# Performance work log

Hardware: AMD Instinct MI355X
Metric: run time of the kernel (lower is better)

## Reference

```python
import jax, jax.numpy as jnp
import numpy as np

HEAD_SIZE = 128


def setup_inputs() -> dict:
    key = jax.random.key(0)
    k0, k1, k2, k3 = jax.random.split(key, 4)
    B, S, E, H = 4, 4096, 1024, HEAD_SIZE
    x = jax.random.normal(k0, (B, S, E), dtype=jnp.float32)
    scale = 1.0 / np.sqrt(E).astype(np.float32)
    Wq = jax.random.normal(k1, (E, H), dtype=jnp.float32) * scale
    Wk = jax.random.normal(k2, (E, H), dtype=jnp.float32) * scale
    Wv = jax.random.normal(k3, (E, H), dtype=jnp.float32) * scale
    k_mask = jnp.ones((B, S), dtype=jnp.int32)
    return {"x": x, "Wq": Wq, "Wk": Wk, "Wv": Wv, "k_mask": k_mask}


def reference(x, Wq, Wk, Wv, k_mask):
    # Self-attention path (kv=None), causal=True
    Q = x @ Wq  # [B, S, H]
    K = x @ Wk  # [B, S, H]
    V = x @ Wv  # [B, S, H]
    inv_sqrt_h = np.float32(1.0 / np.sqrt(HEAD_SIZE))
    att = jnp.einsum('bqh,bkh->bqk', Q, K) * inv_sqrt_h  # [B, S, S]
    neg_inf = jnp.float32(-jnp.inf)
    # padding mask over keys: [B, 1, S_k]
    att = jnp.where(k_mask[:, None, :] == 0, neg_inf, att)
    # causal mask: tril over (q_len, k_len)
    S = Q.shape[1]
    c_mask = jnp.tril(jnp.ones((S, S), dtype=bool))  # [S, S]
    att = jnp.where(c_mask[None, :, :], att, neg_inf)
    att = jax.nn.softmax(att, axis=-1)
    return att @ V  # [B, S, H]
```

## Files before the change

kernel.cpp:

```cpp
#include <hip/hip_runtime.h>
#include <hip/hip_bf16.h>

typedef unsigned short u16;
typedef __attribute__((ext_vector_type(8))) short bf16x8;
typedef __attribute__((ext_vector_type(4))) float f32x4;
typedef __attribute__((ext_vector_type(4))) unsigned short u16x4;

#define SQ 4096
#define HQ 128
#define NCHUNK 144

__device__ __forceinline__ u16 f2b(float f) {
  unsigned int u = __float_as_uint(f);
  unsigned int r = (u + 0x7fffu + ((u >> 16) & 1u)) >> 16;
  return (u16)r;
}

__device__ __forceinline__ u16 f2b_fast(float f) {
  __hip_bfloat16 h = __float2bfloat16(f);
  return __builtin_bit_cast(u16, h);
}

__device__ __forceinline__ float b2f(u16 v) {
  unsigned int u = ((unsigned int)v) << 16;
  return __uint_as_float(u);
}

__device__ __forceinline__ void gload_lds16(const u16* gsrc, u16* ldst) {
  __builtin_amdgcn_global_load_lds((const __attribute__((address_space(1))) void*)gsrc,
                                   (__attribute__((address_space(3))) void*)ldst, 16, 0, 0);
}

__global__ __launch_bounds__(256) void k_wt(const float* __restrict__ Wq, const float* __restrict__ Wk,
                                            const float* __restrict__ Wv, u16* __restrict__ wt) {
  int idx = blockIdx.x * 256 + threadIdx.x;
  int z = idx >> 17, r = idx & 131071, n = r >> 10, k = r & 1023;
  const float* W = (z == 0) ? Wq : (z == 1) ? Wk : Wv;
  wt[idx] = f2b(W[k * 128 + n]);
}

__global__ __launch_bounds__(512, 4) void k_proj(const float* __restrict__ x, const u16* __restrict__ wt,
                                                 u16* __restrict__ qb, u16* __restrict__ kb,
                                                 u16* __restrict__ vt) {
  int mt = blockIdx.x, nh = blockIdx.y;
  int t = threadIdx.x;
  int w = t >> 6, lane = t & 63;
  int wm = w >> 2, wn = w & 3;
  int lr = lane & 15, lg = lane >> 4;

  __shared__ __align__(16) u16 xl[2][64 * 32];
  __shared__ __align__(16) u16 wl[2][192 * 32];

  int srow = t >> 3, sc8 = t & 7;
  const float* xg = x + (long)(mt * 64 + srow) * 1024 + sc8 * 4;
  int xch = ((sc8 >> 1) ^ ((srow >> 1) & 3));
  int xoff = srow * 32 + xch * 8 + (sc8 & 1) * 4;

  f32x4 acc[2][3];
#pragma unroll
  for (int i = 0; i < 2; ++i)
#pragma unroll
    for (int j = 0; j < 3; ++j) acc[i][j] = (f32x4){0.f, 0.f, 0.f, 0.f};

  const u16* wbase = wt + (long)(nh * 192) * 1024;

  auto stage_w = [&](int bufi, int k0) {
#pragma unroll
    for (int i = 0; i < 2; ++i) {
      int ci = i * 512 + t;
      if (ci < 768) {
        int row = ci >> 2, ch = ci & 3;
        gload_lds16(wbase + (long)row * 1024 + k0 + ((ch ^ ((row >> 1) & 3)) << 3),
                    &wl[bufi][0] + ci * 8);
      }
    }
  };

  auto xwrite = [&](int bufi, float4 a, float4 b2) {
    u16x4 o0, o1;
    o0[0] = f2b_fast(a.x); o0[1] = f2b_fast(a.y); o0[2] = f2b_fast(a.z); o0[3] = f2b_fast(a.w);
    o1[0] = f2b_fast(b2.x); o1[1] = f2b_fast(b2.y); o1[2] = f2b_fast(b2.z); o1[3] = f2b_fast(b2.w);
    *(u16x4*)(&xl[bufi][0] + xoff) = (sc8 & 1) ? o0 : o0;
  };

  {
    float4 a0 = *(const float4*)(xg);
    stage_w(0, 0);
    u16x4 o;
    o[0] = f2b_fast(a0.x); o[1] = f2b_fast(a0.y); o[2] = f2b_fast(a0.z); o[3] = f2b_fast(a0.w);
    *(u16x4*)(&xl[0][0] + xoff) = o;
  }
  float4 p0 = *(const float4*)(xg + 32);
  float4 p1 = *(const float4*)(xg + 64);
  __syncthreads();

  for (int ks = 0; ks < 32; ++ks) {
    int cur = ks & 1;
    float4 p2;
    if (ks + 3 < 32) p2 = *(const float4*)(xg + (ks + 3) * 32);
    if (ks + 1 < 32) {
      stage_w(cur ^ 1, (ks + 1) * 32);
      u16x4 o;
      o[0] = f2b_fast(p0.x); o[1] = f2b_fast(p0.y); o[2] = f2b_fast(p0.z); o[3] = f2b_fast(p0.w);
      *(u16x4*)(&xl[cur ^ 1][0] + xoff) = o;
    }
    bf16x8 af[2], bfr[3];
#pragma unroll
    for (int i = 0; i < 2; ++i) {
      int row = wm * 32 + i * 16 + lr;
      af[i] = *(const bf16x8*)(&xl[cur][0] + row * 32 + ((lg ^ ((row >> 1) & 3)) << 3));
    }
#pragma unroll
    for (int j = 0; j < 3; ++j) {
      int row = wn * 48 + j * 16 + lr;
      bfr[j] = *(const bf16x8*)(&wl[cur][0] + row * 32 + ((lg ^ ((row >> 1) & 3)) << 3));
    }
#pragma unroll
    for (int i = 0; i < 2; ++i)
#pragma unroll
      for (int j = 0; j < 3; ++j)
        acc[i][j] = __builtin_amdgcn_mfma_f32_16x16x32_bf16(af[i], bfr[j], acc[i][j], 0, 0, 0);
    p0 = p1; p1 = p2;
    __syncthreads();
  }

#pragma unroll
  for (int i = 0; i < 2; ++i)
#pragma unroll
    for (int j = 0; j < 3; ++j)
#pragma unroll
      for (int r = 0; r < 4; ++r) {
        int m = mt * 64 + wm * 32 + i * 16 + lg * 4 + r;
        int col = nh * 192 + wn * 48 + j * 16 + lr;
        int z = col >> 7, cz = col & 127;
        u16 v = f2b(acc[i][j][r]);
        if (z == 0) qb[(long)m * 128 + cz] = v;
        else if (z == 1) kb[(long)m * 128 + cz] = v;
        else { int bb = m >> 12, sR = m & 4095; vt[(long)bb * 524288 + (long)cz * 4096 + sR] = v; }
      }
}

__global__ __launch_bounds__(512, 4) void k_attn(const u16* __restrict__ qb, const u16* __restrict__ kb,
                                                 const u16* __restrict__ vt, const int* __restrict__ kmask,
                                                 u16* __restrict__ po, float* __restrict__ pl) {
  const float SCALE_LOG2 = 0.08838834764831845f * 1.4426950408889634f;
  const float MFIX = 24.0f;
  int f = (NCHUNK - 1) - (int)blockIdx.x;
  int b = blockIdx.y;
  int qt2 = 0, cum = 0;
  while (cum + ((qt2 + 4) >> 2) <= f) { cum += (qt2 + 4) >> 2; ++qt2; }
  int kc = f - cum;
  int ntile = 2 * qt2 + 2;
  int kt0 = kc * 8;
  int kt1 = min(kt0 + 8, ntile);

  int t = threadIdx.x, w = t >> 6, lane = t & 63;
  int lr = lane & 15, lg = lane >> 4, sw = lr & 7;
  int qrow0 = qt2 * 128 + w * 16;
  const u16* Q = qb + ((long)(b * SQ + qrow0)) * HQ;
  const u16* K = kb + (long)b * SQ * HQ;
  const u16* V = vt + (long)b * HQ * SQ;
  const int* msk = kmask + b * SQ;

  __shared__ __align__(16) u16 Kl[2][64 * 128];
  __shared__ __align__(16) u16 Vl[2][128 * 64];
  __shared__ __align__(16) u16 plds[8][16 * 64];

  bf16x8 aq[4];
#pragma unroll
  for (int c = 0; c < 4; ++c) aq[c] = *(const bf16x8*)(Q + lr * HQ + c * 32 + lg * 8);

  bf16x8 ones;
#pragma unroll
  for (int e = 0; e < 8; ++e) ones[e] = (short)0x3F80;

  f32x4 o[8];
#pragma unroll
  for (int n = 0; n < 8; ++n) o[n] = (f32x4){0.f, 0.f, 0.f, 0.f};
  f32x4 l_acc = (f32x4){0.f, 0.f, 0.f, 0.f};

  auto stage = [&](int bufi, int kb0) {
    const u16* Kg = K + (long)kb0 * HQ;
    const u16* Vg = V + kb0;
#pragma unroll
    for (int i = 0; i < 2; ++i) {
      int ci = w * 2 + i;
      int o16 = ci * 64 + lane;
      int row = o16 >> 4, ch = o16 & 15;
      gload_lds16(Kg + row * HQ + ((ch ^ (row & 7)) << 3), &Kl[bufi][ci * 512]);
    }
#pragma unroll
    for (int i = 0; i < 2; ++i) {
      int ci = w * 2 + i;
      int o16 = ci * 64 + lane;
      int row = o16 >> 3, ch = o16 & 7;
      gload_lds16(Vg + (long)row * SQ + ((ch ^ (row & 7)) << 3), &Vl[bufi][ci * 512]);
    }
  };

  stage(0, kt0 * 64);
  __syncthreads();

  u16* pw = &plds[w][0];
  for (int kt = kt0; kt < kt1; ++kt) {
    int cur = (kt - kt0) & 1;
    int kb0 = kt * 64;
    if (kt + 1 < kt1) stage(cur ^ 1, kb0 + 64);

    if (kb0 <= qrow0 + 15) {
      f32x4 s[4];
#pragma unroll
      for (int h = 0; h < 4; ++h) {
        f32x4 acc = (f32x4){0.f, 0.f, 0.f, 0.f};
        const u16* Kp = &Kl[cur][(h * 16 + lr) * 128];
#pragma unroll
        for (int c = 0; c < 4; ++c) {
          bf16x8 bk = *(const bf16x8*)(Kp + (((c * 4 + lg) ^ sw) << 3));
          acc = __builtin_amdgcn_mfma_f32_16x16x32_bf16(aq[c], bk, acc, 0, 0, 0);
        }
        s[h] = acc;
      }
      float mf[4];
#pragma unroll
      for (int h = 0; h < 4; ++h) mf[h] = (msk[kb0 + h * 16 + lr] != 0) ? 1.0f : 0.0f;
      bool needc = (kb0 + 63 > qrow0);
#pragma unroll
      for (int r = 0; r < 4; ++r) {
        int row = lg * 4 + r;
        int qr = qrow0 + row;
#pragma unroll
        for (int h = 0; h < 4; ++h) {
          float p = __builtin_exp2f(fmaf(s[h][r], SCALE_LOG2, -MFIX)) * mf[h];
          if (needc) p = ((kb0 + h * 16 + lr) <= qr) ? p : 0.0f;
          int poff = row * 64 + ((((h * 2 + (lr >> 3)) ^ (row & 7))) << 3) + (lr & 7);
          pw[poff] = f2b_fast(p);
        }
      }
      bf16x8 ap0 = *(const bf16x8*)(pw + lr * 64 + ((lg ^ sw) << 3));
      bf16x8 ap1 = *(const bf16x8*)(pw + lr * 64 + (((4 + lg) ^ sw) << 3));
      l_acc = __builtin_amdgcn_mfma_f32_16x16x32_bf16(ap0, ones, l_acc, 0, 0, 0);
      l_acc = __builtin_amdgcn_mfma_f32_16x16x32_bf16(ap1, ones, l_acc, 0, 0, 0);
#pragma unroll
      for (int n = 0; n < 8; ++n) {
        const u16* Vp = &Vl[cur][(n * 16 + lr) * 64];
        bf16x8 bv0 = *(const bf16x8*)(Vp + ((lg ^ sw) << 3));
        bf16x8 bv1 = *(const bf16x8*)(Vp + (((4 + lg) ^ sw) << 3));
        o[n] = __builtin_amdgcn_mfma_f32_16x16x32_bf16(ap0, bv0, o[n], 0, 0, 0);
        o[n] = __builtin_amdgcn_mfma_f32_16x16x32_bf16(ap1, bv1, o[n], 0, 0, 0);
      }
    }
    __syncthreads();
  }

  long p = (long)b * NCHUNK + f;
  u16* pob = po + p * 16384;
#pragma unroll
  for (int n = 0; n < 8; ++n)
#pragma unroll
    for (int r = 0; r < 4; ++r)
      pob[(w * 16 + lg * 4 + r) * 128 + n * 16 + lr] = f2b_fast(o[n][r]);
  if (lr == 0) {
#pragma unroll
    for (int r = 0; r < 4; ++r) pl[p * 128 + w * 16 + lg * 4 + r] = l_acc[r];
  }
}

__global__ __launch_bounds__(256) void k_merge(const u16* __restrict__ po, const float* __restrict__ pl,
                                               float* __restrict__ out) {
  int qt2 = blockIdx.x, b = blockIdx.y;
  int nch = (qt2 + 4) >> 2;
  int pre = 0;
  for (int q = 0; q < qt2; ++q) pre += (q + 4) >> 2;
  long pbase = (long)b * NCHUNK + pre;
  int t = threadIdx.x;
  int row = t >> 1, c0 = (t & 1) * 64;
  float l = 0.f;
  for (int i = 0; i < nch; ++i) l += pl[(pbase + i) * 128 + row];
  float inv = 1.0f / l;
  const u16* p0 = po + pbase * 16384 + row * 128 + c0;
  float* orow = out + ((long)(b * SQ + qt2 * 128 + row)) * HQ + c0;
#pragma unroll
  for (int j = 0; j < 64; j += 4) {
    float acc0 = 0.f, acc1 = 0.f, acc2 = 0.f, acc3 = 0.f;
    for (int i = 0; i < nch; ++i) {
      u16x4 v = *(const u16x4*)(p0 + (long)i * 16384 + j);
      acc0 += b2f(v[0]); acc1 += b2f(v[1]); acc2 += b2f(v[2]); acc3 += b2f(v[3]);
    }
    float4 r = {acc0 * inv, acc1 * inv, acc2 * inv, acc3 * inv};
    *(float4*)(orow + j) = r;
  }
}

extern "C" void kernel_launch(void* const* d_in, const int* in_sizes, int n_in,
                              void* d_out, int out_size, void* d_ws, size_t ws_size,
                              hipStream_t stream) {
  const float* x  = (const float*)d_in[0];
  const float* Wq = (const float*)d_in[1];
  const float* Wk = (const float*)d_in[2];
  const float* Wv = (const float*)d_in[3];
  const int* kmask = (const int*)d_in[4];
  char* ws = (char*)d_ws;
  u16* wt = (u16*)(ws + 33554432);
  u16* qb = (u16*)(ws + 34340864);
  u16* kb = (u16*)(ws + 38535168);
  u16* vt = (u16*)(ws + 42729472);
  u16* po = (u16*)ws;
  float* pl = (float*)(ws + 31195136);
  float* out = (float*)d_out;

  k_wt<<<1536, 256, 0, stream>>>(Wq, Wk, Wv, wt);
  k_proj<<<dim3(256, 2), 512, 0, stream>>>(x, wt, qb, kb, vt);
  k_attn<<<dim3(NCHUNK, 4), 512, 0, stream>>>(qb, kb, vt, kmask, po, pl);
  k_merge<<<dim3(32, 4), 256, 0, stream>>>(po, pl, out);
}
```

Baseline: 117.4 us.

## Enlarge projection M-tile to 128 rows and single-buffer attention K/V staging

The projection kernel now processes 128 rows of x per block instead of 64, with each wave computing a 64x48 tile (4x3 MFMA accumulators). This reuses each staged weight tile across twice as many rows and halves the number of projection blocks. The x prefetch depth drops from three stages to two, and each thread now writes 8 bf16 values at once. Separately, the attention kernel drops K/V double buffering in favour of stage-then-sync each tile and relaxes the launch bound. This cuts LDS use per block but exposes load latency, since loads are no longer overlapped with compute.

```diff
diff --git a/kernel.cpp b/kernel.cpp
--- a/kernel.cpp
+++ b/kernel.cpp
@@ -5,6 +5,7 @@
 typedef __attribute__((ext_vector_type(8))) short bf16x8;
 typedef __attribute__((ext_vector_type(4))) float f32x4;
 typedef __attribute__((ext_vector_type(4))) unsigned short u16x4;
+typedef __attribute__((ext_vector_type(8))) unsigned short u16v8;
 
 #define SQ 4096
 #define HQ 128
@@ -48,17 +49,17 @@
   int wm = w >> 2, wn = w & 3;
   int lr = lane & 15, lg = lane >> 4;
 
-  __shared__ __align__(16) u16 xl[2][64 * 32];
+  __shared__ __align__(16) u16 xl[2][128 * 32];
   __shared__ __align__(16) u16 wl[2][192 * 32];
 
-  int srow = t >> 3, sc8 = t & 7;
-  const float* xg = x + (long)(mt * 64 + srow) * 1024 + sc8 * 4;
-  int xch = ((sc8 >> 1) ^ ((srow >> 1) & 3));
-  int xoff = srow * 32 + xch * 8 + (sc8 & 1) * 4;
-
-  f32x4 acc[2][3];
-#pragma unroll
-  for (int i = 0; i < 2; ++i)
+  int srow = t >> 2, g0 = t & 3;
+  const float* xg = x + (long)(mt * 128 + srow) * 1024 + g0 * 8;
+  int xch = g0 ^ ((srow >> 1) & 3);
+  int xoff = srow * 32 + xch * 8;
+
+  f32x4 acc[4][3];
+#pragma unroll
+  for (int i = 0; i < 4; ++i)
 #pragma unroll
     for (int j = 0; j < 3; ++j) acc[i][j] = (f32x4){0.f, 0.f, 0.f, 0.f};
 
@@ -76,38 +77,38 @@
     }
   };
 
-  auto xwrite = [&](int bufi, float4 a, float4 b2) {
-    u16x4 o0, o1;
-    o0[0] = f2b_fast(a.x); o0[1] = f2b_fast(a.y); o0[2] = f2b_fast(a.z); o0[3] = f2b_fast(a.w);
-    o1[0] = f2b_fast(b2.x); o1[1] = f2b_fast(b2.y); o1[2] = f2b_fast(b2.z); o1[3] = f2b_fast(b2.w);
-    *(u16x4*)(&xl[bufi][0] + xoff) = (sc8 & 1) ? o0 : o0;
+  auto xwrite = [&](int bufi, float4 a, float4 b) {
+    u16v8 o;
+    o[0] = f2b_fast(a.x); o[1] = f2b_fast(a.y); o[2] = f2b_fast(a.z); o[3] = f2b_fast(a.w);
+    o[4] = f2b_fast(b.x); o[5] = f2b_fast(b.y); o[6] = f2b_fast(b.z); o[7] = f2b_fast(b.w);
+    *(u16v8*)(&xl[bufi][0] + xoff) = o;
   };
 
   {
     float4 a0 = *(const float4*)(xg);
+    float4 a1 = *(const float4*)(xg + 4);
     stage_w(0, 0);
-    u16x4 o;
-    o[0] = f2b_fast(a0.x); o[1] = f2b_fast(a0.y); o[2] = f2b_fast(a0.z); o[3] = f2b_fast(a0.w);
-    *(u16x4*)(&xl[0][0] + xoff) = o;
-  }
-  float4 p0 = *(const float4*)(xg + 32);
-  float4 p1 = *(const float4*)(xg + 64);
+    xwrite(0, a0, a1);
+  }
+  float4 p0a = *(const float4*)(xg + 32);
+  float4 p0b = *(const float4*)(xg + 36);
   __syncthreads();
 
   for (int ks = 0; ks < 32; ++ks) {
     int cur = ks & 1;
-    float4 p2;
-    if (ks + 3 < 32) p2 = *(const float4*)(xg + (ks + 3) * 32);
+    float4 p1a, p1b;
+    if (ks + 2 < 32) {
+      p1a = *(const float4*)(xg + (ks + 2) * 32);
+      p1b = *(const float4*)(xg + (ks + 2) * 32 + 4);
+    }
     if (ks + 1 < 32) {
       stage_w(cur ^ 1, (ks + 1) * 32);
-      u16x4 o;
-      o[0] = f2b_fast(p0.x); o[1] = f2b_fast(p0.y); o[2] = f2b_fast(p0.z); o[3] = f2b_fast(p0.w);
-      *(u16x4*)(&xl[cur ^ 1][0] + xoff) = o;
-    }
-    bf16x8 af[2], bfr[3];
-#pragma unroll
-    for (int i = 0; i < 2; ++i) {
-      int row = wm * 32 + i * 16 + lr;
+      xwrite(cur ^ 1, p0a, p0b);
+    }
+    bf16x8 af[4], bfr[3];
+#pragma unroll
+    for (int i = 0; i < 4; ++i) {
+      int row = wm * 64 + i * 16 + lr;
       af[i] = *(const bf16x8*)(&xl[cur][0] + row * 32 + ((lg ^ ((row >> 1) & 3)) << 3));
     }
 #pragma unroll
@@ -116,21 +117,21 @@
       bfr[j] = *(const bf16x8*)(&wl[cur][0] + row * 32 + ((lg ^ ((row >> 1) & 3)) << 3));
     }
 #pragma unroll
-    for (int i = 0; i < 2; ++i)
+    for (int i = 0; i < 4; ++i)
 #pragma unroll
       for (int j = 0; j < 3; ++j)
         acc[i][j] = __builtin_amdgcn_mfma_f32_16x16x32_bf16(af[i], bfr[j], acc[i][j], 0, 0, 0);
-    p0 = p1; p1 = p2;
+    p0a = p1a; p0b = p1b;
     __syncthreads();
   }
 
 #pragma unroll
-  for (int i = 0; i < 2; ++i)
+  for (int i = 0; i < 4; ++i)
 #pragma unroll
     for (int j = 0; j < 3; ++j)
 #pragma unroll
       for (int r = 0; r < 4; ++r) {
-        int m = mt * 64 + wm * 32 + i * 16 + lg * 4 + r;
+        int m = mt * 128 + wm * 64 + i * 16 + lg * 4 + r;
         int col = nh * 192 + wn * 48 + j * 16 + lr;
         int z = col >> 7, cz = col & 127;
         u16 v = f2b(acc[i][j][r]);
@@ -140,9 +141,9 @@
       }
 }
 
-__global__ __launch_bounds__(512, 4) void k_attn(const u16* __restrict__ qb, const u16* __restrict__ kb,
-                                                 const u16* __restrict__ vt, const int* __restrict__ kmask,
-                                                 u16* __restrict__ po, float* __restrict__ pl) {
+__global__ __launch_bounds__(512) void k_attn(const u16* __restrict__ qb, const u16* __restrict__ kb,
+                                              const u16* __restrict__ vt, const int* __restrict__ kmask,
+                                              u16* __restrict__ po, float* __restrict__ pl) {
   const float SCALE_LOG2 = 0.08838834764831845f * 1.4426950408889634f;
   const float MFIX = 24.0f;
   int f = (NCHUNK - 1) - (int)blockIdx.x;
@@ -162,8 +163,8 @@
   const u16* V = vt + (long)b * HQ * SQ;
   const int* msk = kmask + b * SQ;
 
-  __shared__ __align__(16) u16 Kl[2][64 * 128];
-  __shared__ __align__(16) u16 Vl[2][128 * 64];
+  __shared__ __align__(16) u16 Kl[64 * 128];
+  __shared__ __align__(16) u16 Vl[128 * 64];
   __shared__ __align__(16) u16 plds[8][16 * 64];
 
   bf16x8 aq[4];
@@ -179,7 +180,7 @@
   for (int n = 0; n < 8; ++n) o[n] = (f32x4){0.f, 0.f, 0.f, 0.f};
   f32x4 l_acc = (f32x4){0.f, 0.f, 0.f, 0.f};
 
-  auto stage = [&](int bufi, int kb0) {
+  auto stage = [&](int kb0) {
     const u16* Kg = K + (long)kb0 * HQ;
     const u16* Vg = V + kb0;
 #pragma unroll
@@ -187,32 +188,29 @@
       int ci = w * 2 + i;
       int o16 = ci * 64 + lane;
       int row = o16 >> 4, ch = o16 & 15;
-      gload_lds16(Kg + row * HQ + ((ch ^ (row & 7)) << 3), &Kl[bufi][ci * 512]);
+      gload_lds16(Kg + row * HQ + ((ch ^ (row & 7)) << 3), &Kl[ci * 512]);
     }
 #pragma unroll
     for (int i = 0; i < 2; ++i) {
       int ci = w * 2 + i;
       int o16 = ci * 64 + lane;
       int row = o16 >> 3, ch = o16 & 7;
-      gload_lds16(Vg + (long)row * SQ + ((ch ^ (row & 7)) << 3), &Vl[bufi][ci * 512]);
+      gload_lds16(Vg + (long)row * SQ + ((ch ^ (row & 7)) << 3), &Vl[ci * 512]);
     }
   };
-
-  stage(0, kt0 * 64);
-  __syncthreads();
 
   u16* pw = &plds[w][0];
   for (int kt = kt0; kt < kt1; ++kt) {
-    int cur = (kt - kt0) & 1;
     int kb0 = kt * 64;
-    if (kt + 1 < kt1) stage(cur ^ 1, kb0 + 64);
+    stage(kb0);
+    __syncthreads();
 
     if (kb0 <= qrow0 + 15) {
       f32x4 s[4];
 #pragma unroll
       for (int h = 0; h < 4; ++h) {
         f32x4 acc = (f32x4){0.f, 0.f, 0.f, 0.f};
-        const u16* Kp = &Kl[cur][(h * 16 + lr) * 128];
+        const u16* Kp = &Kl[(h * 16 + lr) * 128];
 #pragma unroll
         for (int c = 0; c < 4; ++c) {
           bf16x8 bk = *(const bf16x8*)(Kp + (((c * 4 + lg) ^ sw) << 3));
@@ -242,7 +240,7 @@
       l_acc = __builtin_amdgcn_mfma_f32_16x16x32_bf16(ap1, ones, l_acc, 0, 0, 0);
 #pragma unroll
       for (int n = 0; n < 8; ++n) {
-        const u16* Vp = &Vl[cur][(n * 16 + lr) * 64];
+        const u16* Vp = &Vl[(n * 16 + lr) * 64];
         bf16x8 bv0 = *(const bf16x8*)(Vp + ((lg ^ sw) << 3));
         bf16x8 bv1 = *(const bf16x8*)(Vp + (((4 + lg) ^ sw) << 3));
         o[n] = __builtin_amdgcn_mfma_f32_16x16x32_bf16(ap0, bv0, o[n], 0, 0, 0);
@@ -309,7 +307,7 @@
   float* out = (float*)d_out;
 
   k_wt<<<1536, 256, 0, stream>>>(Wq, Wk, Wv, wt);
-  k_proj<<<dim3(256, 2), 512, 0, stream>>>(x, wt, qb, kb, vt);
+  k_proj<<<dim3(128, 2), 512, 0, stream>>>(x, wt, qb, kb, vt);
   k_attn<<<dim3(NCHUNK, 4), 512, 0, stream>>>(qb, kb, vt, kmask, po, pl);
   k_merge<<<dim3(32, 4), 256, 0, stream>>>(po, pl, out);
 }
```

New measurement: 137.2 us. +16.8%, slower.
